# Performance work log

Measured on AMD Instinct MI355X. Metric: run time of the kernel, lower is better.

## Reference

```python
import jax, jax.numpy as jnp
import numpy as np

ZETA = 1.1
GAMMA = -0.1

B, F, D = 1024, 32, 128


def setup_inputs() -> dict:
    key = jax.random.key(0)
    k1, k2 = jax.random.split(key)
    feature = jax.random.normal(k1, (B, F, D), dtype=jnp.float32)
    # nn.Parameter init: normal(mean=0, std=0.001)
    matrix = jax.random.normal(k2, (F, F, D, D), dtype=jnp.float32) * 0.001
    return {"feature": feature, "matrix": matrix}


def reference(feature, matrix):
    # feature: [B, F, D]; matrix (logAlpha of hard-concrete gate): [F, F, D, D]
    nF = matrix.shape[0]
    # strict upper-triangular pair mask over (i, j)
    mask = jnp.triu(jnp.ones((nF, nF), dtype=feature.dtype), k=1)
    # deterministic (eval-mode) hard-concrete gate: stretch + clamp
    s = jax.nn.sigmoid(matrix)
    z = jnp.clip(s * (ZETA - GAMMA) + GAMMA, 0.0, 1.0)
    l0_out = mask[:, :, None, None] * z  # [F, F, D, D]
    # out[b,i,j] = f_i^T Z_ij f_j  == sum_{d,e} f[b,i,d] * Z[i,j,d,e] * f[b,j,e]
    # (faithful to: (f[:, :, None, :, None] @ f[:, None, :, None, :]) * Z, summed over (d, e))
    out = jnp.einsum('bid,ijde,bje->bij', feature, l0_out, feature)
    return out
```

## Files before the change

kernel.cpp:

```cpp
#include <hip/hip_runtime.h>

#define B_SZ 1024
#define F_SZ 32
#define D_SZ 128
#define FD   4096
#define NPAIR 496

typedef __bf16 bf16x8 __attribute__((ext_vector_type(8)));
typedef float floatx4 __attribute__((ext_vector_type(4)));
typedef unsigned short u16x8 __attribute__((ext_vector_type(8)));

__device__ __forceinline__ unsigned short f2bf(float f) {
  unsigned u = __float_as_uint(f);
  u += 0x7fffu + ((u >> 16) & 1u);
  return (unsigned short)(u >> 16);
}

__device__ __forceinline__ float bf2f(unsigned short h) {
  return __uint_as_float(((unsigned)h) << 16);
}

__device__ __forceinline__ void gload_lds16(const void* g, void* l) {
  __builtin_amdgcn_global_load_lds(
      (const __attribute__((address_space(1))) unsigned int*)g,
      (__attribute__((address_space(3))) unsigned int*)l,
      16, 0, 0);
}

__global__ __launch_bounds__(256)
void prep_kernel(const float* __restrict__ feat, const float* __restrict__ mat,
                 unsigned short* __restrict__ featB,
                 unsigned short* __restrict__ ZT, float* __restrict__ out) {
  const int bid = blockIdx.x, t = threadIdx.x;
  __shared__ unsigned short tr[128 * 72];

  if (bid < 2 * NPAIR) {
    const int pid = bid >> 1, h = bid & 1, d0 = h * 64;
    int p = pid, i = 0;
    while (p >= F_SZ - 1 - i) { p -= F_SZ - 1 - i; ++i; }
    const int j = i + 1 + p;
    const float* zp = mat + (((size_t)i * F_SZ + j) * (size_t)(D_SZ * D_SZ));
    #pragma unroll
    for (int it = 0; it < 8; ++it) {
      int idx4 = it * 256 + t;
      int dl = idx4 >> 5, e4 = (idx4 & 31) * 4;
      const float4 v = *(const float4*)(zp + (size_t)(d0 + dl) * D_SZ + e4);
      float zs[4] = {v.x, v.y, v.z, v.w};
      #pragma unroll
      for (int c = 0; c < 4; ++c) {
        float s = 1.0f / (1.0f + __expf(-zs[c]));
        float z = fminf(1.0f, fmaxf(0.0f, fmaf(s, 1.2f, -0.1f)));
        tr[(e4 + c) * 72 + dl] = f2bf(z);
      }
    }
    __syncthreads();
    #pragma unroll
    for (int it = 0; it < 4; ++it) {
      int G = it * 256 + t;
      int e = G >> 3, gl = G & 7;
      int gs = gl ^ (e & 7);
      u16x8 v = *(const u16x8*)&tr[e * 72 + gs * 8];
      *(u16x8*)&ZT[(size_t)pid * (D_SZ * D_SZ) + e * 128 + d0 + gl * 8] = v;
    }
  } else if (bid < 2 * NPAIR + 1024) {
    int idx = (bid - 2 * NPAIR) * 256 + t;
    const float4* f4 = (const float4*)feat + (size_t)idx * 4;
    #pragma unroll
    for (int q = 0; q < 2; ++q) {
      float4 a = f4[q * 2], b = f4[q * 2 + 1];
      float vs[8] = {a.x, a.y, a.z, a.w, b.x, b.y, b.z, b.w};
      u16x8 hi;
      #pragma unroll
      for (int c = 0; c < 8; ++c) hi[c] = f2bf(vs[c]);
      *(u16x8*)&featB[(size_t)idx * 16 + q * 8] = hi;
    }
  } else {
    int idx = (bid - (2 * NPAIR + 1024)) * 256 + t;
    float4* o4 = (float4*)out + (size_t)idx * 4;
    float4 z = {0.f, 0.f, 0.f, 0.f};
    o4[0] = z; o4[1] = z; o4[2] = z; o4[3] = z;
  }
}

__global__ __launch_bounds__(256, 2)
void interaction_pair_kernel(const unsigned short* __restrict__ featB,
                             const unsigned short* __restrict__ ZT,
                             float* __restrict__ out) {
  __shared__ unsigned short sZ[128 * 128];

  const int t    = threadIdx.x;
  const int w    = t >> 6;
  const int lane = t & 63;
  const int l15  = lane & 15;
  const int quad = lane >> 4;
  const int swz  = (l15 & 7) << 4;

  const int bid  = blockIdx.x;
  const int work = (bid & 7) * 248 + (bid >> 3);
  const int pid   = work >> 2;
  const int split = work & 3;
  int p = pid, i = 0;
  while (p >= F_SZ - 1 - i) { p -= F_SZ - 1 - i; ++i; }
  const int j = i + 1 + p;

  {
    const char* src = (const char*)(ZT + (size_t)pid * (D_SZ * D_SZ));
    #pragma unroll
    for (int it = 0; it < 8; ++it) {
      int off = it * 4096 + w * 1024;
      gload_lds16(src + off + lane * 16, (char*)sZ + off);
    }
  }
  __syncthreads();

  #pragma unroll 1
  for (int pass = 0; pass < 2; ++pass) {
    const int rbase = split * 256 + pass * 128 + w * 32;

    floatx4 acc[8][2];
    #pragma unroll
    for (int m = 0; m < 8; ++m) {
      acc[m][0] = (floatx4){0.f, 0.f, 0.f, 0.f};
      acc[m][1] = (floatx4){0.f, 0.f, 0.f, 0.f};
    }

    const unsigned short* bp0 = featB + (size_t)(rbase + l15) * FD + i * D_SZ + quad * 8;
    const unsigned short* bp1 = bp0 + (size_t)16 * FD;
    #pragma unroll
    for (int k0 = 0; k0 < 4; ++k0) {
      bf16x8 b0 = *(const bf16x8*)(bp0 + k0 * 32);
      bf16x8 b1 = *(const bf16x8*)(bp1 + k0 * 32);
      #pragma unroll
      for (int m = 0; m < 8; ++m) {
        bf16x8 za = *(const bf16x8*)((const char*)sZ + (m * 16 + l15) * 256 +
                                     ((k0 * 64 + quad * 16) ^ swz));
        acc[m][0] = __builtin_amdgcn_mfma_f32_16x16x32_bf16(za, b0, acc[m][0], 0, 0, 0);
        acc[m][1] = __builtin_amdgcn_mfma_f32_16x16x32_bf16(za, b1, acc[m][1], 0, 0, 0);
      }
    }

    #pragma unroll
    for (int n = 0; n < 2; ++n) {
      const int row = rbase + n * 16 + l15;
      const unsigned short* fj = featB + (size_t)row * FD + j * D_SZ + quad * 4;
      float pl = 0.f;
      #pragma unroll
      for (int m = 0; m < 8; ++m) {
        const ushort4 hv = *(const ushort4*)(fj + m * 16);
        floatx4 c = acc[m][n];
        pl += c[0] * bf2f(hv.x) + c[1] * bf2f(hv.y)
            + c[2] * bf2f(hv.z) + c[3] * bf2f(hv.w);
      }
      pl += __shfl_xor(pl, 16, 64);
      pl += __shfl_xor(pl, 32, 64);
      if (quad == 0)
        out[(size_t)row * (F_SZ * F_SZ) + (size_t)i * F_SZ + j] = pl;
    }
  }
}

extern "C" void kernel_launch(void* const* d_in, const int* in_sizes, int n_in,
                              void* d_out, int out_size, void* d_ws, size_t ws_size,
                              hipStream_t stream) {
  const float* feat = (const float*)d_in[0];
  const float* mat  = (const float*)d_in[1];
  float* out = (float*)d_out;

  unsigned short* featB = (unsigned short*)d_ws;
  unsigned short* ZT    = featB + (size_t)B_SZ * F_SZ * D_SZ;

  const int prep_grid = 2 * NPAIR + 1024 + 256;
  prep_kernel<<<dim3(prep_grid), dim3(256), 0, stream>>>(feat, mat, featB, ZT, out);
  interaction_pair_kernel<<<dim3(NPAIR * 4), dim3(256), 0, stream>>>(featB, ZT, out);
}
```

Measured before the change: 155.0 us.

## Prefetch feature operands into registers before LDS barrier and drop XCD block remap

Loads the f_i and f_j feature fragments for the first row pass into registers before the Z tile lands in LDS. It issues the second pass's loads before the first pass computes, so global latency overlaps the barrier and the MFMA work. It also replaces the XCD-aware block-to-work mapping with a plain linear mapping. The change raises register pressure, with about 48 extra VGPRs of prefetched data under a 2-blocks-per-SIMD launch bound, and changes L2 locality for the Z tiles.

Result: no change. 153.5 us (-1.0%).

```diff
diff --git a/kernel.cpp b/kernel.cpp
--- a/kernel.cpp
+++ b/kernel.cpp
@@ -82,6 +82,39 @@
   }
 }
 
+#define DO_PASS(FI, FJ, RB)                                                    \
+  {                                                                            \
+    floatx4 acc[8][2];                                                         \
+    _Pragma("unroll") for (int m = 0; m < 8; ++m) {                            \
+      acc[m][0] = (floatx4){0.f, 0.f, 0.f, 0.f};                               \
+      acc[m][1] = (floatx4){0.f, 0.f, 0.f, 0.f};                               \
+    }                                                                          \
+    _Pragma("unroll") for (int k0 = 0; k0 < 4; ++k0) {                         \
+      _Pragma("unroll") for (int m = 0; m < 8; ++m) {                          \
+        bf16x8 za = *(const bf16x8*)((const char*)sZ + (m * 16 + l15) * 256 +  \
+                                     ((k0 * 64 + quad * 16) ^ swz));           \
+        acc[m][0] = __builtin_amdgcn_mfma_f32_16x16x32_bf16(za, FI[k0],        \
+                                                            acc[m][0], 0, 0, 0);\
+        acc[m][1] = __builtin_amdgcn_mfma_f32_16x16x32_bf16(za, FI[4 + k0],    \
+                                                            acc[m][1], 0, 0, 0);\
+      }                                                                        \
+    }                                                                          \
+    _Pragma("unroll") for (int n = 0; n < 2; ++n) {                            \
+      float pl = 0.f;                                                          \
+      _Pragma("unroll") for (int m = 0; m < 8; ++m) {                          \
+        const ushort4 hv = FJ[n * 8 + m];                                      \
+        const floatx4 c = acc[m][n];                                           \
+        pl += c[0] * bf2f(hv.x) + c[1] * bf2f(hv.y)                            \
+            + c[2] * bf2f(hv.z) + c[3] * bf2f(hv.w);                           \
+      }                                                                        \
+      pl += __shfl_xor(pl, 16, 64);                                            \
+      pl += __shfl_xor(pl, 32, 64);                                            \
+      if (quad == 0)                                                           \
+        out[(size_t)(RB + n * 16 + l15) * (F_SZ * F_SZ) +                      \
+            (size_t)i * F_SZ + j] = pl;                                        \
+    }                                                                          \
+  }
+
 __global__ __launch_bounds__(256, 2)
 void interaction_pair_kernel(const unsigned short* __restrict__ featB,
                              const unsigned short* __restrict__ ZT,
@@ -95,14 +128,34 @@
   const int quad = lane >> 4;
   const int swz  = (l15 & 7) << 4;
 
-  const int bid  = blockIdx.x;
-  const int work = (bid & 7) * 248 + (bid >> 3);
-  const int pid   = work >> 2;
-  const int split = work & 3;
+  const int bid   = blockIdx.x;
+  const int pid   = bid >> 2;
+  const int split = bid & 3;
   int p = pid, i = 0;
   while (p >= F_SZ - 1 - i) { p -= F_SZ - 1 - i; ++i; }
   const int j = i + 1 + p;
 
+  const int rb0 = split * 256 + w * 32;
+  const int rb1 = rb0 + 128;
+
+  bf16x8 fiA[8];
+  ushort4 fjA[16];
+  {
+    const unsigned short* bp = featB + (size_t)(rb0 + l15) * FD + i * D_SZ + quad * 8;
+    #pragma unroll
+    for (int k0 = 0; k0 < 4; ++k0) {
+      fiA[k0]     = *(const bf16x8*)(bp + k0 * 32);
+      fiA[4 + k0] = *(const bf16x8*)(bp + (size_t)16 * FD + k0 * 32);
+    }
+    #pragma unroll
+    for (int n = 0; n < 2; ++n) {
+      const unsigned short* fj =
+          featB + (size_t)(rb0 + n * 16 + l15) * FD + j * D_SZ + quad * 4;
+      #pragma unroll
+      for (int m = 0; m < 8; ++m) fjA[n * 8 + m] = *(const ushort4*)(fj + m * 16);
+    }
+  }
+
   {
     const char* src = (const char*)(ZT + (size_t)pid * (D_SZ * D_SZ));
     #pragma unroll
@@ -113,50 +166,27 @@
   }
   __syncthreads();
 
-  #pragma unroll 1
-  for (int pass = 0; pass < 2; ++pass) {
-    const int rbase = split * 256 + pass * 128 + w * 32;
-
-    floatx4 acc[8][2];
-    #pragma unroll
-    for (int m = 0; m < 8; ++m) {
-      acc[m][0] = (floatx4){0.f, 0.f, 0.f, 0.f};
-      acc[m][1] = (floatx4){0.f, 0.f, 0.f, 0.f};
-    }
-
-    const unsigned short* bp0 = featB + (size_t)(rbase + l15) * FD + i * D_SZ + quad * 8;
-    const unsigned short* bp1 = bp0 + (size_t)16 * FD;
+  bf16x8 fiB[8];
+  ushort4 fjB[16];
+  {
+    const unsigned short* bp = featB + (size_t)(rb1 + l15) * FD + i * D_SZ + quad * 8;
     #pragma unroll
     for (int k0 = 0; k0 < 4; ++k0) {
-      bf16x8 b0 = *(const bf16x8*)(bp0 + k0 * 32);
-      bf16x8 b1 = *(const bf16x8*)(bp1 + k0 * 32);
-      #pragma unroll
-      for (int m = 0; m < 8; ++m) {
-        bf16x8 za = *(const bf16x8*)((const char*)sZ + (m * 16 + l15) * 256 +
-                                     ((k0 * 64 + quad * 16) ^ swz));
-        acc[m][0] = __builtin_amdgcn_mfma_f32_16x16x32_bf16(za, b0, acc[m][0], 0, 0, 0);
-        acc[m][1] = __builtin_amdgcn_mfma_f32_16x16x32_bf16(za, b1, acc[m][1], 0, 0, 0);
-      }
-    }
-
+      fiB[k0]     = *(const bf16x8*)(bp + k0 * 32);
+      fiB[4 + k0] = *(const bf16x8*)(bp + (size_t)16 * FD + k0 * 32);
+    }
     #pragma unroll
     for (int n = 0; n < 2; ++n) {
-      const int row = rbase + n * 16 + l15;
-      const unsigned short* fj = featB + (size_t)row * FD + j * D_SZ + quad * 4;
-      float pl = 0.f;
-      #pragma unroll
-      for (int m = 0; m < 8; ++m) {
-        const ushort4 hv = *(const ushort4*)(fj + m * 16);
-        floatx4 c = acc[m][n];
-        pl += c[0] * bf2f(hv.x) + c[1] * bf2f(hv.y)
-            + c[2] * bf2f(hv.z) + c[3] * bf2f(hv.w);
-      }
-      pl += __shfl_xor(pl, 16, 64);
-      pl += __shfl_xor(pl, 32, 64);
-      if (quad == 0)
-        out[(size_t)row * (F_SZ * F_SZ) + (size_t)i * F_SZ + j] = pl;
-    }
-  }
+      const unsigned short* fj =
+          featB + (size_t)(rb1 + n * 16 + l15) * FD + j * D_SZ + quad * 4;
+      #pragma unroll
+      for (int m = 0; m < 8; ++m) fjB[n * 8 + m] = *(const ushort4*)(fj + m * 16);
+    }
+  }
+
+  DO_PASS(fiA, fjA, rb0);
+
+  DO_PASS(fiB, fjB, rb1);
 }
 
 extern "C" void kernel_launch(void* const* d_in, const int* in_sizes, int n_in,
```
